# Kernel optimization log

Measured on AMD Instinct MI355X. Metric: run time of the kernel, lower is better.

The kernel has to match this reference:

```python
import jax, jax.numpy as jnp
import numpy as np

N_EMBD = 1024
N_HEAD = 16
HEAD_DIM = N_EMBD // N_HEAD


def setup_inputs() -> dict:
    key = jax.random.key(0)
    ks = jax.random.split(key, 9)
    B, T, C = 2, 2048, N_EMBD
    s = 1.0 / np.sqrt(C)
    x = jax.random.normal(ks[0], (B, T, C), dtype=jnp.float32)
    Wk = jax.random.normal(ks[1], (C, C), dtype=jnp.float32) * s
    bk = jnp.zeros((C,), dtype=jnp.float32)
    Wq = jax.random.normal(ks[2], (C, C), dtype=jnp.float32) * s
    bq = jnp.zeros((C,), dtype=jnp.float32)
    Wv = jax.random.normal(ks[3], (C, C), dtype=jnp.float32) * s
    bv = jnp.zeros((C,), dtype=jnp.float32)
    Wp = jax.random.normal(ks[4], (C, C), dtype=jnp.float32) * s
    bp = jnp.zeros((C,), dtype=jnp.float32)
    return {"x": x, "Wk": Wk, "bk": bk, "Wq": Wq, "bq": bq,
            "Wv": Wv, "bv": bv, "Wp": Wp, "bp": bp}


def reference(x, Wk, bk, Wq, bq, Wv, bv, Wp, bp):
    B, T, C = x.shape
    H, D = N_HEAD, HEAD_DIM
    # torch Linear: y = x @ W.T + b
    k = (x @ Wk.T + bk).reshape(B, T, H, D)  # [B,T,H,D]
    q = (x @ Wq.T + bq).reshape(B, T, H, D)
    v = (x @ Wv.T + bv).reshape(B, T, H, D)
    scale = 1.0 / jnp.sqrt(jnp.asarray(D, dtype=x.dtype))
    scores = jnp.einsum('bqhd,bkhd->bhqk', q, k) * scale  # [B,H,T,T]
    w = jax.nn.softmax(scores, axis=-1)
    attn = jnp.einsum('bhqk,bkhd->bqhd', w, v).reshape(B, T, C)
    return attn @ Wp.T + bp
```

## Files before the change

kernel.cpp:

```cpp
#include <hip/hip_runtime.h>
#include <hip/hip_bf16.h>
#include <stdint.h>

#define TT 2048
#define CC 1024
#define NH 16
#define HD 64
#define QKVN 3072

typedef __attribute__((ext_vector_type(8))) short short8;
typedef __attribute__((ext_vector_type(4))) float floatx4;
typedef __attribute__((ext_vector_type(4))) unsigned short ushortx4;

typedef const __attribute__((address_space(1))) void gas_void;
typedef __attribute__((address_space(3))) void las_void;

__device__ __forceinline__ void gload16(const void* g, void* l) {
  __builtin_amdgcn_global_load_lds((gas_void*)g, (las_void*)l, 16, 0, 0);
}

__device__ __forceinline__ unsigned short f2bf(float f) {
  union { float f; uint32_t u; } v; v.f = f;
  uint32_t u = v.u;
  uint32_t r = (u + 0x7fffu + ((u >> 16) & 1u)) >> 16;
  return (unsigned short)r;
}

__device__ __forceinline__ float fexp2(float x) {
#if __has_builtin(__builtin_amdgcn_exp2f)
  return __builtin_amdgcn_exp2f(x);
#else
  return exp2f(x);
#endif
}

#define QSCALE 0.18033688011112042f

__device__ __forceinline__ int perm64(int t) {
  const int kk = t >> 5, r5 = t & 31;
  const int g = ((r5 >> 3) & 2) | ((r5 >> 2) & 1);
  const int slot = (r5 & 3) | ((r5 >> 1) & 4);
  return kk * 32 + g * 8 + slot;
}

__global__ __launch_bounds__(256) void cvt_fused(const float* __restrict__ x,
                                                 const float* __restrict__ wq,
                                                 const float* __restrict__ wk,
                                                 const float* __restrict__ wv,
                                                 const float* __restrict__ wp,
                                                 unsigned short* __restrict__ xb,
                                                 unsigned short* __restrict__ wqkvb,
                                                 unsigned short* __restrict__ wpb) {
  const int i = blockIdx.x * blockDim.x + threadIdx.x;
  if (i < 1048576) {
    const float4 v = reinterpret_cast<const float4*>(x)[i];
    ushortx4 o; o[0] = f2bf(v.x); o[1] = f2bf(v.y); o[2] = f2bf(v.z); o[3] = f2bf(v.w);
    reinterpret_cast<ushortx4*>(xb)[i] = o;
    return;
  }
  const int j = i - 1048576;
  const int seg = j >> 18;
  const int idx = j & 262143;
  const float* src = (seg == 0) ? wq : (seg == 1) ? wk : (seg == 2) ? wv : wp;
  const float sc = (seg == 0) ? QSCALE : 1.0f;
  const float4 v = reinterpret_cast<const float4*>(src)[idx];
  ushortx4 o;
  o[0] = f2bf(v.x * sc); o[1] = f2bf(v.y * sc); o[2] = f2bf(v.z * sc); o[3] = f2bf(v.w * sc);
  if (seg < 3)
    reinterpret_cast<ushortx4*>(wqkvb)[j] = o;
  else
    reinterpret_cast<ushortx4*>(wpb)[idx] = o;
}

__global__ __launch_bounds__(512) void gemm_qkv(const unsigned short* __restrict__ A,
                                                const unsigned short* __restrict__ W,
                                                const float* __restrict__ b0,
                                                const float* __restrict__ b1,
                                                const float* __restrict__ b2,
                                                unsigned short* __restrict__ out,
                                                unsigned short* __restrict__ Vt) {
  __shared__ unsigned short lsA[2][256 * 64];
  __shared__ unsigned short lsB[2][256 * 64];
  const int tid = threadIdx.x;
  const int wave = tid >> 6, lane = tid & 63;
  const int g = lane >> 4, c16 = lane & 15;
  const int m0 = blockIdx.y * 256, n0 = blockIdx.x * 256;
  const int wm = (wave >> 2) * 128, wn = (wave & 3) * 64;

  floatx4 acc[8][4];
#pragma unroll
  for (int i = 0; i < 8; ++i)
#pragma unroll
    for (int j = 0; j < 4; ++j) acc[i][j] = (floatx4){0.f, 0.f, 0.f, 0.f};

  const int srow = lane >> 3, sj = lane & 7;

  auto stage2 = [&](int buf, int kt, int rho) {
    const int kb = wave * 4 + rho;
    const int r = kb * 8 + srow;
    const int gj = (sj ^ (r & 7)) << 3;
    gload16(A + (size_t)(m0 + r) * CC + kt + gj, (char*)lsA[buf] + kb * 1024);
    gload16(W + (size_t)(n0 + r) * CC + kt + gj, (char*)lsB[buf] + kb * 1024);
  };

#pragma unroll
  for (int rho = 0; rho < 4; ++rho) stage2(0, 0, rho);
  asm volatile("s_waitcnt vmcnt(0)" ::: "memory");
  __builtin_amdgcn_s_barrier();

#pragma unroll 2
  for (int t = 0; t < 16; ++t) {
    const int buf = t & 1;
    const char* la = (const char*)lsA[buf];
    const char* lb = (const char*)lsB[buf];
    const bool pre = (t < 15);
#pragma unroll
    for (int p = 0; p < 4; ++p) {
      const int ih = (p >> 1) * 4;
      const int jh = (p & 1) * 2;
      short8 af[4][2], bfr[2][2];
#pragma unroll
      for (int i = 0; i < 4; ++i) {
        const int ra = wm + (ih + i) * 16 + c16;
#pragma unroll
        for (int kk = 0; kk < 2; ++kk) {
          const int ca = (kk * 4 + g) ^ (ra & 7);
          af[i][kk] = *reinterpret_cast<const short8*>(la + ra * 128 + (ca << 4));
        }
      }
#pragma unroll
      for (int j = 0; j < 2; ++j) {
        const int rb = wn + (jh + j) * 16 + c16;
#pragma unroll
        for (int kk = 0; kk < 2; ++kk) {
          const int cb = (kk * 4 + g) ^ (rb & 7);
          bfr[j][kk] = *reinterpret_cast<const short8*>(lb + rb * 128 + (cb << 4));
        }
      }
      if (pre && p < 2) {
        stage2(buf ^ 1, (t + 1) * 64, 2 * p);
        stage2(buf ^ 1, (t + 1) * 64, 2 * p + 1);
      }
      __builtin_amdgcn_s_barrier();
      asm volatile("s_waitcnt lgkmcnt(0)" ::: "memory");
      __builtin_amdgcn_sched_barrier(0);
      __builtin_amdgcn_s_setprio(1);
#pragma unroll
      for (int kk = 0; kk < 2; ++kk)
#pragma unroll
        for (int i = 0; i < 4; ++i)
#pragma unroll
          for (int j = 0; j < 2; ++j)
            acc[ih + i][jh + j] = __builtin_amdgcn_mfma_f32_16x16x32_bf16(
                af[i][kk], bfr[j][kk], acc[ih + i][jh + j], 0, 0, 0);
      __builtin_amdgcn_s_setprio(0);
      if (p == 3 && pre)
        asm volatile("s_waitcnt vmcnt(0)" ::: "memory");
      __builtin_amdgcn_s_barrier();
    }
  }

  const int rgrp = g * 4;
  const float* bias = (n0 < 1024) ? b0 : (n0 < 2048 ? b1 : b2);
  const float bsc = (n0 < 1024) ? QSCALE : 1.0f;

  if (n0 >= 2048) {
#pragma unroll
    for (int i = 0; i < 8; ++i) {
      const int tk0 = m0 + wm + i * 16 + rgrp;
      const int bb = tk0 >> 11;
      const int tw = tk0 & 2047;
      const int tpos = (tw & ~63) + perm64(tw & 63);
#pragma unroll
      for (int j = 0; j < 4; ++j) {
        const int vdim = n0 - 2048 + wn + j * 16 + c16;
        const int h = vdim >> 6, d = vdim & 63;
        const float bv = bias[vdim];
        ushortx4 ov;
#pragma unroll
        for (int r = 0; r < 4; ++r) ov[r] = f2bf(acc[i][j][r] + bv);
        *reinterpret_cast<ushortx4*>(
            &Vt[((size_t)((bb * NH + h) * HD + d)) * TT + tpos]) = ov;
      }
    }
    return;
  }

#pragma unroll
  for (int i = 0; i < 8; ++i) {
    const int gm0 = m0 + wm + i * 16 + rgrp;
#pragma unroll
    for (int j = 0; j < 4; ++j) {
      const int gn = n0 + wn + j * 16 + c16;
      const float bv = bias[gn & 1023] * bsc;
#pragma unroll
      for (int r = 0; r < 4; ++r)
        out[(size_t)(gm0 + r) * QKVN + gn] = f2bf(acc[i][j][r] + bv);
    }
  }
}

__global__ __launch_bounds__(256) void gemm_proj(const unsigned short* __restrict__ A,
                                                 const unsigned short* __restrict__ W,
                                                 const float* __restrict__ bias,
                                                 float* __restrict__ outv) {
  __shared__ unsigned short lsA[128 * 64];
  __shared__ unsigned short lsB[128 * 64];
  const int tid = threadIdx.x;
  const int wave = tid >> 6, lane = tid & 63;
  const int m0 = blockIdx.y * 128, n0 = blockIdx.x * 128;
  const int wm = (wave >> 1) * 64, wn = (wave & 1) * 64;
  const int K = CC, N = CC;

  floatx4 acc[4][4];
#pragma unroll
  for (int i = 0; i < 4; ++i)
#pragma unroll
    for (int j = 0; j < 4; ++j)
      acc[i][j] = (floatx4){0.f, 0.f, 0.f, 0.f};

  const int sr = lane >> 3;
  const int sj = lane & 7;

  for (int kt = 0; kt < K; kt += 64) {
    __syncthreads();
#pragma unroll
    for (int t = 0; t < 4; ++t) {
      const int g4 = wave * 4 + t;
      const int r = g4 * 8 + sr;
      const int gj = (sj ^ (r & 7)) << 3;
      gload16(A + (size_t)(m0 + r) * K + kt + gj, (char*)lsA + g4 * 1024);
      gload16(W + (size_t)(n0 + r) * K + kt + gj, (char*)lsB + g4 * 1024);
    }
    __syncthreads();

#pragma unroll
    for (int kk = 0; kk < 2; ++kk) {
      short8 af[4], bfr[4];
#pragma unroll
      for (int i = 0; i < 4; ++i) {
        const int ra = wm + i * 16 + (lane & 15);
        const int ca = (kk * 4 + (lane >> 4)) ^ (ra & 7);
        af[i] = *reinterpret_cast<const short8*>((const char*)lsA + ra * 128 + (ca << 4));
        const int rb = wn + i * 16 + (lane & 15);
        const int cb = (kk * 4 + (lane >> 4)) ^ (rb & 7);
        bfr[i] = *reinterpret_cast<const short8*>((const char*)lsB + rb * 128 + (cb << 4));
      }
#pragma unroll
      for (int i = 0; i < 4; ++i)
#pragma unroll
        for (int j = 0; j < 4; ++j)
          acc[i][j] = __builtin_amdgcn_mfma_f32_16x16x32_bf16(af[i], bfr[j], acc[i][j], 0, 0, 0);
    }
  }

  const int col = lane & 15;
  const int rgrp = (lane >> 4) * 4;
#pragma unroll
  for (int i = 0; i < 4; ++i) {
    const int gm0 = m0 + wm + i * 16 + rgrp;
#pragma unroll
    for (int j = 0; j < 4; ++j) {
      const int gn = n0 + wn + j * 16 + col;
      const float bv = bias[gn];
#pragma unroll
      for (int r = 0; r < 4; ++r)
        outv[(size_t)(gm0 + r) * N + gn] = acc[i][j][r] + bv;
    }
  }
}

__global__ __launch_bounds__(256) void attn_fwd(const unsigned short* __restrict__ QKV,
                                                const unsigned short* __restrict__ Vt,
                                                unsigned short* __restrict__ Ob) {
  __shared__ unsigned short lsK[2][64 * 64];
  __shared__ unsigned short lsV[2][64 * 64];
  const int tid = threadIdx.x;
  const int wave = tid >> 6, lane = tid & 63;
  const int g = lane >> 4;
  const int c16 = lane & 15;
  const int bh = blockIdx.x;
  const int b = bh >> 4, h = bh & 15;
  const int q0 = blockIdx.y * 64 + wave * 16;

  short8 qf[2];
  {
    const unsigned short* qp =
        QKV + (size_t)(b * TT + q0 + c16) * QKVN + h * HD + g * 8;
    qf[0] = *reinterpret_cast<const short8*>(qp);
    qf[1] = *reinterpret_cast<const short8*>(qp + 32);
  }

  short8 ones;
#pragma unroll
  for (int i = 0; i < 8; ++i) ones[i] = (short)0x3F80;

  floatx4 o[4];
#pragma unroll
  for (int f = 0; f < 4; ++f) o[f] = (floatx4){0.f, 0.f, 0.f, 0.f};
  floatx4 lacc = (floatx4){0.f, 0.f, 0.f, 0.f};

  const int sr = lane >> 3, sj = lane & 7;

  auto stage = [&](int buf, int kt) {
#pragma unroll
    for (int t = 0; t < 2; ++t) {
      const int g8 = wave * 2 + t;
      const int r = g8 * 8 + sr;
      const int gj = (sj ^ (r & 7)) << 3;
      gload16(QKV + (size_t)(b * TT + kt + r) * QKVN + CC + h * HD + gj,
              (char*)lsK[buf] + g8 * 1024);
      gload16(Vt + ((size_t)bh * HD + r) * TT + kt + gj, (char*)lsV[buf] + g8 * 1024);
    }
  };

  auto compute = [&](const unsigned short* lk, const unsigned short* lv) {
    floatx4 s[4];
#pragma unroll
    for (int cb = 0; cb < 4; ++cb) s[cb] = (floatx4){0.f, 0.f, 0.f, 0.f};
    __builtin_amdgcn_s_setprio(1);
#pragma unroll
    for (int kk = 0; kk < 2; ++kk) {
#pragma unroll
      for (int cb = 0; cb < 4; ++cb) {
        const int rk = cb * 16 + c16;
        const int ck = (kk * 4 + g) ^ (rk & 7);
        const short8 kf =
            *reinterpret_cast<const short8*>((const char*)lk + rk * 128 + (ck << 4));
        s[cb] = __builtin_amdgcn_mfma_f32_16x16x32_bf16(kf, qf[kk], s[cb], 0, 0, 0);
      }
    }
    __builtin_amdgcn_s_setprio(0);

    unsigned int w[4][2];
#pragma unroll
    for (int cb = 0; cb < 4; ++cb) {
#pragma unroll
      for (int r = 0; r < 4; ++r) s[cb][r] = fexp2(s[cb][r]);
      asm("v_cvt_pk_bf16_f32 %0, %1, %2"
          : "=v"(w[cb][0]) : "v"(s[cb][0]), "v"(s[cb][1]));
      asm("v_cvt_pk_bf16_f32 %0, %1, %2"
          : "=v"(w[cb][1]) : "v"(s[cb][2]), "v"(s[cb][3]));
    }

#pragma unroll
    for (int kk = 0; kk < 2; ++kk) {
      unsigned int pa0 = w[2 * kk][0], pb0 = w[2 * kk + 1][0];
      unsigned int pa1 = w[2 * kk][1], pb1 = w[2 * kk + 1][1];
      asm("v_permlane32_swap_b32 %0, %1" : "+v"(pa0), "+v"(pb0));
      asm("v_permlane32_swap_b32 %0, %1" : "+v"(pa1), "+v"(pb1));
      union { unsigned int u[4]; short8 v; } pk;
      pk.u[0] = pa0; pk.u[1] = pa1; pk.u[2] = pb0; pk.u[3] = pb1;
      const short8 pbv = pk.v;
      __builtin_amdgcn_s_setprio(1);
#pragma unroll
      for (int f = 0; f < 4; ++f) {
        const int rv = f * 16 + c16;
        const int cv = (4 * kk + g) ^ (rv & 7);
        const short8 vf =
            *reinterpret_cast<const short8*>((const char*)lv + rv * 128 + (cv << 4));
        o[f] = __builtin_amdgcn_mfma_f32_16x16x32_bf16(vf, pbv, o[f], 0, 0, 0);
      }
      lacc = __builtin_amdgcn_mfma_f32_16x16x32_bf16(ones, pbv, lacc, 0, 0, 0);
      __builtin_amdgcn_s_setprio(0);
    }
  };

  stage(0, 0);

#pragma unroll 2
  for (int it = 0; it < TT / 64; ++it) {
    const int buf = it & 1;
    if (it < TT / 64 - 1) {
      stage(buf ^ 1, (it + 1) * 64);
      asm volatile("s_waitcnt vmcnt(4)" ::: "memory");
    } else {
      asm volatile("s_waitcnt vmcnt(0)" ::: "memory");
    }
    __builtin_amdgcn_s_barrier();
    __builtin_amdgcn_sched_barrier(0);
    compute((const unsigned short*)lsK[buf], (const unsigned short*)lsV[buf]);
    __builtin_amdgcn_s_barrier();
  }

  {
    const float inv = 1.0f / lacc[0];
    const size_t gm = (size_t)(b * TT + q0 + c16) * CC;
#pragma unroll
    for (int f = 0; f < 4; ++f) {
      ushortx4 ov;
#pragma unroll
      for (int r = 0; r < 4; ++r) ov[r] = f2bf(o[f][r] * inv);
      *reinterpret_cast<ushortx4*>(&Ob[gm + h * HD + f * 16 + 4 * g]) = ov;
    }
  }
}

extern "C" void kernel_launch(void* const* d_in, const int* in_sizes, int n_in,
                              void* d_out, int out_size, void* d_ws, size_t ws_size,
                              hipStream_t stream) {
  (void)in_sizes; (void)n_in; (void)out_size; (void)ws_size;
  const float* x  = (const float*)d_in[0];
  const float* Wk = (const float*)d_in[1];
  const float* bk = (const float*)d_in[2];
  const float* Wq = (const float*)d_in[3];
  const float* bq = (const float*)d_in[4];
  const float* Wv = (const float*)d_in[5];
  const float* bv = (const float*)d_in[6];
  const float* Wp = (const float*)d_in[7];
  const float* bp = (const float*)d_in[8];
  float* out = (float*)d_out;

  char* ws = (char*)d_ws;
  const size_t MB = 1u << 20;
  unsigned short* xb    = (unsigned short*)(ws);
  unsigned short* Wqkvb = (unsigned short*)(ws + 8 * MB);
  unsigned short* Wpb   = (unsigned short*)(ws + 14 * MB);
  unsigned short* QKVb  = (unsigned short*)(ws + 16 * MB);
  unsigned short* Vtb   = (unsigned short*)(ws + 40 * MB);
  unsigned short* Ab    = (unsigned short*)(ws + 48 * MB);

  const int M = 2 * TT;

  cvt_fused<<<8192, 256, 0, stream>>>(x, Wq, Wk, Wv, Wp, xb, Wqkvb, Wpb);

  gemm_qkv<<<dim3(QKVN / 256, M / 256), 512, 0, stream>>>(xb, Wqkvb, bq, bk, bv,
                                                          QKVb, Vtb);

  attn_fwd<<<dim3(2 * NH, TT / 64), 256, 0, stream>>>(QKVb, Vtb, Ab);

  gemm_proj<<<dim3(CC / 128, M / 128), 256, 0, stream>>>(Ab, Wpb, bp, out);
}
```

Before: 131.0 us.

## Prefetch two K-tiles ahead in QKV and projection GEMMs

The QKV GEMM now issues all loads for a tile two iterations ahead, once per K-step after compute, and waits with vmcnt(8) so one tile stays in flight. This replaces the earlier interleaved per-phase prefetch and removes the barriers between phases. The projection GEMM moves from a single-buffered loop with syncthreads to the same double-buffered scheme with setprio around the MFMA block. This doubles LDS use in the projection kernel, which may reduce occupancy, and it relies on the exact vmcnt accounting being right.

```diff
diff --git a/kernel.cpp b/kernel.cpp
--- a/kernel.cpp
+++ b/kernel.cpp
@@ -95,17 +95,20 @@
 
   const int srow = lane >> 3, sj = lane & 7;
 
-  auto stage2 = [&](int buf, int kt, int rho) {
-    const int kb = wave * 4 + rho;
-    const int r = kb * 8 + srow;
-    const int gj = (sj ^ (r & 7)) << 3;
-    gload16(A + (size_t)(m0 + r) * CC + kt + gj, (char*)lsA[buf] + kb * 1024);
-    gload16(W + (size_t)(n0 + r) * CC + kt + gj, (char*)lsB[buf] + kb * 1024);
+  auto stageT = [&](int buf, int kt) {
+#pragma unroll
+    for (int rho = 0; rho < 4; ++rho) {
+      const int kb = wave * 4 + rho;
+      const int r = kb * 8 + srow;
+      const int gj = (sj ^ (r & 7)) << 3;
+      gload16(A + (size_t)(m0 + r) * CC + kt + gj, (char*)lsA[buf] + kb * 1024);
+      gload16(W + (size_t)(n0 + r) * CC + kt + gj, (char*)lsB[buf] + kb * 1024);
+    }
   };
 
-#pragma unroll
-  for (int rho = 0; rho < 4; ++rho) stage2(0, 0, rho);
-  asm volatile("s_waitcnt vmcnt(0)" ::: "memory");
+  stageT(0, 0);
+  stageT(1, 64);
+  asm volatile("s_waitcnt vmcnt(8)" ::: "memory");
   __builtin_amdgcn_s_barrier();
 
 #pragma unroll 2
@@ -113,7 +116,6 @@
     const int buf = t & 1;
     const char* la = (const char*)lsA[buf];
     const char* lb = (const char*)lsB[buf];
-    const bool pre = (t < 15);
 #pragma unroll
     for (int p = 0; p < 4; ++p) {
       const int ih = (p >> 1) * 4;
@@ -137,11 +139,6 @@
           bfr[j][kk] = *reinterpret_cast<const short8*>(lb + rb * 128 + (cb << 4));
         }
       }
-      if (pre && p < 2) {
-        stage2(buf ^ 1, (t + 1) * 64, 2 * p);
-        stage2(buf ^ 1, (t + 1) * 64, 2 * p + 1);
-      }
-      __builtin_amdgcn_s_barrier();
       asm volatile("s_waitcnt lgkmcnt(0)" ::: "memory");
       __builtin_amdgcn_sched_barrier(0);
       __builtin_amdgcn_s_setprio(1);
@@ -154,8 +151,15 @@
             acc[ih + i][jh + j] = __builtin_amdgcn_mfma_f32_16x16x32_bf16(
                 af[i][kk], bfr[j][kk], acc[ih + i][jh + j], 0, 0, 0);
       __builtin_amdgcn_s_setprio(0);
-      if (p == 3 && pre)
+    }
+    if (t < 15) {
+      __builtin_amdgcn_s_barrier();
+      if (t < 14) {
+        stageT(buf, (t + 2) * 64);
+        asm volatile("s_waitcnt vmcnt(8)" ::: "memory");
+      } else {
         asm volatile("s_waitcnt vmcnt(0)" ::: "memory");
+      }
       __builtin_amdgcn_s_barrier();
     }
   }
@@ -204,8 +208,8 @@
                                                  const unsigned short* __restrict__ W,
                                                  const float* __restrict__ bias,
                                                  float* __restrict__ outv) {
-  __shared__ unsigned short lsA[128 * 64];
-  __shared__ unsigned short lsB[128 * 64];
+  __shared__ unsigned short lsA[2][128 * 64];
+  __shared__ unsigned short lsB[2][128 * 64];
   const int tid = threadIdx.x;
   const int wave = tid >> 6, lane = tid & 63;
   const int m0 = blockIdx.y * 128, n0 = blockIdx.x * 128;
@@ -222,35 +226,61 @@
   const int sr = lane >> 3;
   const int sj = lane & 7;
 
-  for (int kt = 0; kt < K; kt += 64) {
-    __syncthreads();
+  auto stageT = [&](int buf, int kt) {
 #pragma unroll
     for (int t = 0; t < 4; ++t) {
       const int g4 = wave * 4 + t;
       const int r = g4 * 8 + sr;
       const int gj = (sj ^ (r & 7)) << 3;
-      gload16(A + (size_t)(m0 + r) * K + kt + gj, (char*)lsA + g4 * 1024);
-      gload16(W + (size_t)(n0 + r) * K + kt + gj, (char*)lsB + g4 * 1024);
-    }
-    __syncthreads();
-
-#pragma unroll
-    for (int kk = 0; kk < 2; ++kk) {
-      short8 af[4], bfr[4];
-#pragma unroll
-      for (int i = 0; i < 4; ++i) {
-        const int ra = wm + i * 16 + (lane & 15);
+      gload16(A + (size_t)(m0 + r) * K + kt + gj, (char*)lsA[buf] + g4 * 1024);
+      gload16(W + (size_t)(n0 + r) * K + kt + gj, (char*)lsB[buf] + g4 * 1024);
+    }
+  };
+
+  stageT(0, 0);
+  stageT(1, 64);
+  asm volatile("s_waitcnt vmcnt(8)" ::: "memory");
+  __builtin_amdgcn_s_barrier();
+
+#pragma unroll 2
+  for (int t = 0; t < 16; ++t) {
+    const int buf = t & 1;
+    const char* la = (const char*)lsA[buf];
+    const char* lb = (const char*)lsB[buf];
+    short8 af[4][2], bfr[4][2];
+#pragma unroll
+    for (int i = 0; i < 4; ++i) {
+      const int ra = wm + i * 16 + (lane & 15);
+      const int rb = wn + i * 16 + (lane & 15);
+#pragma unroll
+      for (int kk = 0; kk < 2; ++kk) {
         const int ca = (kk * 4 + (lane >> 4)) ^ (ra & 7);
-        af[i] = *reinterpret_cast<const short8*>((const char*)lsA + ra * 128 + (ca << 4));
-        const int rb = wn + i * 16 + (lane & 15);
         const int cb = (kk * 4 + (lane >> 4)) ^ (rb & 7);
-        bfr[i] = *reinterpret_cast<const short8*>((const char*)lsB + rb * 128 + (cb << 4));
-      }
+        af[i][kk] = *reinterpret_cast<const short8*>(la + ra * 128 + (ca << 4));
+        bfr[i][kk] = *reinterpret_cast<const short8*>(lb + rb * 128 + (cb << 4));
+      }
+    }
+    asm volatile("s_waitcnt lgkmcnt(0)" ::: "memory");
+    __builtin_amdgcn_sched_barrier(0);
+    __builtin_amdgcn_s_setprio(1);
+#pragma unroll
+    for (int kk = 0; kk < 2; ++kk)
 #pragma unroll
       for (int i = 0; i < 4; ++i)
 #pragma unroll
         for (int j = 0; j < 4; ++j)
-          acc[i][j] = __builtin_amdgcn_mfma_f32_16x16x32_bf16(af[i], bfr[j], acc[i][j], 0, 0, 0);
+          acc[i][j] = __builtin_amdgcn_mfma_f32_16x16x32_bf16(af[i][kk], bfr[j][kk],
+                                                              acc[i][j], 0, 0, 0);
+    __builtin_amdgcn_s_setprio(0);
+    if (t < 15) {
+      __builtin_amdgcn_s_barrier();
+      if (t < 14) {
+        stageT(buf, (t + 2) * 64);
+        asm volatile("s_waitcnt vmcnt(8)" ::: "memory");
+      } else {
+        asm volatile("s_waitcnt vmcnt(0)" ::: "memory");
+      }
+      __builtin_amdgcn_s_barrier();
     }
   }
 
```

Measured after the change: 127.2 us. 3.0% less time.
